# Kernel tuning notes

Measured on AMD Instinct MI355X. Metric: run time of the kernel, lower is better.

## Reference

```python
import jax, jax.numpy as jnp
import numpy as np


def setup_inputs() -> dict:
    key = jax.random.key(0)
    k1, k2 = jax.random.split(key)
    # x: [B, C, H, W] with C == embedding_dim
    x = jax.random.normal(k1, (32, 64, 64, 64), dtype=jnp.float32)
    # codebook: [num_embeddings, embedding_dim] (nn.Embedding weight)
    codebook = jax.random.normal(k2, (512, 64), dtype=jnp.float32) * 0.05
    return {"x": x, "codebook": codebook}


def reference(x, codebook):
    # VQ.forward: permute NCHW -> NHWC, nearest-codebook indices via
    # ||a-b||^2 = ||a||^2 + ||b||^2 - 2 a.b  (the addmm in torch)
    xt = jnp.transpose(x, (0, 2, 3, 1))            # [B, H, W, D]
    flat = xt.reshape(-1, codebook.shape[1])       # [N, D]
    cb_sqr = jnp.sum(codebook * codebook, axis=1)              # [K]
    in_sqr = jnp.sum(flat * flat, axis=1, keepdims=True)       # [N, 1]
    distances = cb_sqr + in_sqr - 2.0 * (flat @ codebook.T)    # [N, K]
    indices = jnp.argmin(distances, axis=1).reshape(xt.shape[:-1])  # [B, H, W]
    return indices
```

## Files before the change

### kernel.cpp

```cpp
#include <hip/hip_runtime.h>

#define VQ_K 512
#define VQ_D 64
#define VQ_N (32 * 64 * 64)
#define CH_STRIDE 4096
#define B_STRIDE  262144
#define KSPLIT 4
#define KPW (VQ_K / KSPLIT)

__global__ void cb_sqr_kernel(const float* __restrict__ cb,
                              float* __restrict__ cbsq) {
    int k = blockIdx.x * blockDim.x + threadIdx.x;
    if (k < VQ_K) {
        float s = 0.f;
        #pragma unroll
        for (int d = 0; d < VQ_D; ++d) {
            float v = cb[k * VQ_D + d];
            s = fmaf(v, v, s);
        }
        cbsq[k] = s;
    }
}

__global__ __launch_bounds__(256, 4) void vq_argmin_kernel(
        const float* __restrict__ x,
        const float* __restrict__ cb,
        const float* __restrict__ cbsq,
        int* __restrict__ out) {
    int t   = threadIdx.x;
    int pos = t & 63;
    int w   = __builtin_amdgcn_readfirstlane(t >> 6);
    int n   = blockIdx.x * 64 + pos;
    int b   = n >> 12;
    int p   = n & 4095;
    const float* xb = x + b * B_STRIDE + p;

    float v[VQ_D];
    #pragma unroll
    for (int d = 0; d < VQ_D; ++d) v[d] = xb[d * CH_STRIDE];
    #pragma unroll
    for (int d = 0; d < VQ_D; ++d) asm volatile("" : "+v"(v[d]));

    float s0 = 0.f, s1 = 0.f, s2 = 0.f, s3 = 0.f;
    #pragma unroll
    for (int d = 0; d < VQ_D; d += 4) {
        s0 = fmaf(v[d + 0], v[d + 0], s0);
        s1 = fmaf(v[d + 1], v[d + 1], s1);
        s2 = fmaf(v[d + 2], v[d + 2], s2);
        s3 = fmaf(v[d + 3], v[d + 3], s3);
    }
    float insq = (s0 + s1) + (s2 + s3);

    float best = 3.4e38f;
    int bi = 0;
    const float* rowbase = cb + w * (KPW * VQ_D);
    const float* sqbase  = cbsq + w * KPW;
    for (int kk = 0; kk < KPW; ++kk) {
        const float* row = rowbase + kk * VQ_D;
        float d0 = 0.f, d1 = 0.f, d2 = 0.f, d3 = 0.f;
        #pragma unroll
        for (int d = 0; d < VQ_D; d += 4) {
            d0 = fmaf(v[d + 0], row[d + 0], d0);
            d1 = fmaf(v[d + 1], row[d + 1], d1);
            d2 = fmaf(v[d + 2], row[d + 2], d2);
            d3 = fmaf(v[d + 3], row[d + 3], d3);
        }
        float dot  = (d0 + d1) + (d2 + d3);
        float dist = (insq + sqbase[kk]) - 2.f * dot;
        if (dist < best) { best = dist; bi = w * KPW + kk; }
    }

    __shared__ float sbest[KSPLIT][64];
    __shared__ int   sbi[KSPLIT][64];
    sbest[w][pos] = best;
    sbi[w][pos]   = bi;
    __syncthreads();
    if (t < 64) {
        float bb = sbest[0][t];
        int   ii = sbi[0][t];
        #pragma unroll
        for (int j = 1; j < KSPLIT; ++j) {
            float c = sbest[j][t];
            if (c < bb) { bb = c; ii = sbi[j][t]; }
        }
        out[blockIdx.x * 64 + t] = ii;
    }
}

extern "C" void kernel_launch(void* const* d_in, const int* in_sizes, int n_in,
                              void* d_out, int out_size, void* d_ws, size_t ws_size,
                              hipStream_t stream) {
    const float* x  = (const float*)d_in[0];
    const float* cb = (const float*)d_in[1];
    int* out = (int*)d_out;
    float* cbsq = (float*)d_ws;

    cb_sqr_kernel<<<1, VQ_K, 0, stream>>>(cb, cbsq);
    vq_argmin_kernel<<<VQ_N / 64, 256, 0, stream>>>(x, cb, cbsq, out);
}
```

Baseline: 181.1 us.

## Stage input vectors in LDS and block codebook rows by eight per pass

```diff
diff --git a/kernel.cpp b/kernel.cpp
--- a/kernel.cpp
+++ b/kernel.cpp
@@ -7,6 +7,7 @@
 #define B_STRIDE  262144
 #define KSPLIT 4
 #define KPW (VQ_K / KSPLIT)
+#define KB 8
 
 __global__ void cb_sqr_kernel(const float* __restrict__ cb,
                               float* __restrict__ cbsq) {
@@ -22,32 +23,39 @@
     }
 }
 
-__global__ __launch_bounds__(256, 4) void vq_argmin_kernel(
+__global__ __launch_bounds__(256) void vq_argmin_kernel(
         const float* __restrict__ x,
         const float* __restrict__ cb,
         const float* __restrict__ cbsq,
         int* __restrict__ out) {
+    __shared__ float sx[VQ_D][64];
+    __shared__ float sbest[KSPLIT][64];
+    __shared__ int   sbi[KSPLIT][64];
+
     int t   = threadIdx.x;
     int pos = t & 63;
     int w   = __builtin_amdgcn_readfirstlane(t >> 6);
-    int n   = blockIdx.x * 64 + pos;
-    int b   = n >> 12;
-    int p   = n & 4095;
-    const float* xb = x + b * B_STRIDE + p;
+    int n0  = blockIdx.x * 64;
+    int b   = n0 >> 12;
+    int p0  = n0 & 4095;
 
-    float v[VQ_D];
+    const float* xrow = x + b * B_STRIDE + p0;
     #pragma unroll
-    for (int d = 0; d < VQ_D; ++d) v[d] = xb[d * CH_STRIDE];
-    #pragma unroll
-    for (int d = 0; d < VQ_D; ++d) asm volatile("" : "+v"(v[d]));
+    for (int r = 0; r < 16; ++r) {
+        int d = w + r * 4;
+        sx[d][pos] = xrow[d * CH_STRIDE + pos];
+    }
+    __syncthreads();
 
     float s0 = 0.f, s1 = 0.f, s2 = 0.f, s3 = 0.f;
     #pragma unroll
     for (int d = 0; d < VQ_D; d += 4) {
-        s0 = fmaf(v[d + 0], v[d + 0], s0);
-        s1 = fmaf(v[d + 1], v[d + 1], s1);
-        s2 = fmaf(v[d + 2], v[d + 2], s2);
-        s3 = fmaf(v[d + 3], v[d + 3], s3);
+        float v0 = sx[d + 0][pos], v1 = sx[d + 1][pos];
+        float v2 = sx[d + 2][pos], v3 = sx[d + 3][pos];
+        s0 = fmaf(v0, v0, s0);
+        s1 = fmaf(v1, v1, s1);
+        s2 = fmaf(v2, v2, s2);
+        s3 = fmaf(v3, v3, s3);
     }
     float insq = (s0 + s1) + (s2 + s3);
 
@@ -55,23 +63,41 @@
     int bi = 0;
     const float* rowbase = cb + w * (KPW * VQ_D);
     const float* sqbase  = cbsq + w * KPW;
-    for (int kk = 0; kk < KPW; ++kk) {
-        const float* row = rowbase + kk * VQ_D;
-        float d0 = 0.f, d1 = 0.f, d2 = 0.f, d3 = 0.f;
+
+    #pragma unroll 1
+    for (int kb = 0; kb < KPW; kb += KB) {
+        float a0[KB], a1[KB], a2[KB], a3[KB];
         #pragma unroll
-        for (int d = 0; d < VQ_D; d += 4) {
-            d0 = fmaf(v[d + 0], row[d + 0], d0);
-            d1 = fmaf(v[d + 1], row[d + 1], d1);
-            d2 = fmaf(v[d + 2], row[d + 2], d2);
-            d3 = fmaf(v[d + 3], row[d + 3], d3);
+        for (int j = 0; j < KB; ++j) { a0[j] = 0.f; a1[j] = 0.f; a2[j] = 0.f; a3[j] = 0.f; }
+
+        #pragma unroll
+        for (int c = 0; c < 8; ++c) {
+            float xv0 = sx[c * 8 + 0][pos], xv1 = sx[c * 8 + 1][pos];
+            float xv2 = sx[c * 8 + 2][pos], xv3 = sx[c * 8 + 3][pos];
+            float xv4 = sx[c * 8 + 4][pos], xv5 = sx[c * 8 + 5][pos];
+            float xv6 = sx[c * 8 + 6][pos], xv7 = sx[c * 8 + 7][pos];
+            #pragma unroll
+            for (int j = 0; j < KB; ++j) {
+                const float* row = rowbase + (kb + j) * VQ_D + c * 8;
+                a0[j] = fmaf(xv0, row[0], a0[j]);
+                a1[j] = fmaf(xv1, row[1], a1[j]);
+                a2[j] = fmaf(xv2, row[2], a2[j]);
+                a3[j] = fmaf(xv3, row[3], a3[j]);
+                a0[j] = fmaf(xv4, row[4], a0[j]);
+                a1[j] = fmaf(xv5, row[5], a1[j]);
+                a2[j] = fmaf(xv6, row[6], a2[j]);
+                a3[j] = fmaf(xv7, row[7], a3[j]);
+            }
         }
-        float dot  = (d0 + d1) + (d2 + d3);
-        float dist = (insq + sqbase[kk]) - 2.f * dot;
-        if (dist < best) { best = dist; bi = w * KPW + kk; }
+
+        #pragma unroll
+        for (int j = 0; j < KB; ++j) {
+            float dot  = (a0[j] + a1[j]) + (a2[j] + a3[j]);
+            float dist = (insq + sqbase[kb + j]) - 2.f * dot;
+            if (dist < best) { best = dist; bi = w * KPW + kb + j; }
+        }
     }
 
-    __shared__ float sbest[KSPLIT][64];
-    __shared__ int   sbi[KSPLIT][64];
     sbest[w][pos] = best;
     sbi[w][pos]   = bi;
     __syncthreads();
@@ -83,7 +109,7 @@
             float c = sbest[j][t];
             if (c < bb) { bb = c; ii = sbi[j][t]; }
         }
-        out[blockIdx.x * 64 + t] = ii;
+        out[n0 + t] = ii;
     }
 }
 
```

Result: slower. 190.2 us (+5.0%).
